# Optimization experiments

Measured on AMD Instinct MI355X. Metric: run time of the kernel, lower is better.

The kernel has to match this reference:

```python
import jax, jax.numpy as jnp
import numpy as np

N_NODES = 100000
N_EDGES = 1600000
IN_CH = 64
HID = 64
OUT = 2


def sage_conv(x, src, dst, W_agg, W_root, b):
    # PyG SAGEConv (mean aggr): out = lin_l(mean_{j in N(i)} x_j) + lin_r(x_i)
    n = x.shape[0]
    msgs = x[src]                                        # [E, F] gather
    agg = jax.ops.segment_sum(msgs, dst, num_segments=n)  # [N, F] scatter-add
    cnt = jax.ops.segment_sum(jnp.ones((src.shape[0], 1), x.dtype), dst, num_segments=n)
    agg = agg / jnp.maximum(cnt, 1)                      # mean; isolated nodes -> 0
    return agg @ W_agg + x @ W_root + b


def setup_inputs() -> dict:
    key = jax.random.key(0)
    ks = jax.random.split(key, 8)
    s = lambda f: 1.0 / np.sqrt(f)
    x = jax.random.normal(ks[0], (N_NODES, IN_CH), dtype=jnp.float32)
    edge_index = jax.random.randint(ks[1], (2, N_EDGES), 0, N_NODES, dtype=jnp.int64)
    return {
        "x": x,
        "edge_index": edge_index,
        "W1_agg": jax.random.normal(ks[2], (IN_CH, HID), dtype=jnp.float32) * s(IN_CH),
        "W1_root": jax.random.normal(ks[3], (IN_CH, HID), dtype=jnp.float32) * s(IN_CH),
        "b1": jnp.zeros((HID,), jnp.float32),
        "W2_agg": jax.random.normal(ks[4], (HID, HID), dtype=jnp.float32) * s(HID),
        "W2_root": jax.random.normal(ks[5], (HID, HID), dtype=jnp.float32) * s(HID),
        "b2": jnp.zeros((HID,), jnp.float32),
        "W_lin": jax.random.normal(ks[6], (HID, OUT), dtype=jnp.float32) * s(HID),
        "b_lin": jnp.zeros((OUT,), jnp.float32),
    }


def reference(x, edge_index, W1_agg, W1_root, b1, W2_agg, W2_root, b2, W_lin, b_lin):
    src, dst = edge_index[0], edge_index[1]
    h = jax.nn.relu(sage_conv(x, src, dst, W1_agg, W1_root, b1))   # dropout = identity (eval)
    h = jax.nn.relu(sage_conv(h, src, dst, W2_agg, W2_root, b2))
    return h @ W_lin + b_lin
```

## Files before the change

### kernel.cpp

```cpp
#include <hip/hip_runtime.h>
#include <hip/hip_bf16.h>

#define FEAT 64
#define CHUNK 8192
#define MAX_NB 1024

typedef __attribute__((ext_vector_type(8))) short bf16x8;
typedef __attribute__((ext_vector_type(4))) float f32x4;
typedef __attribute__((ext_vector_type(2))) float f32x2;

__device__ __forceinline__ float bflo2f(unsigned int u) {
    union { unsigned int u; float f; } v; v.u = u << 16; return v.f;
}
__device__ __forceinline__ float bfhi2f(unsigned int u) {
    union { unsigned int u; float f; } v; v.u = u & 0xffff0000u; return v.f;
}
__device__ __forceinline__ unsigned short f2bf(float f) {
    union { float f; unsigned int u; } v; v.f = f;
    unsigned int u = v.u;
    u += 0x7fffu + ((u >> 16) & 1u);
    return (unsigned short)(u >> 16);
}
__device__ __forceinline__ f32x2 bfpair(unsigned int u) {
    f32x2 r; r.x = bflo2f(u & 0xffffu); r.y = bfhi2f(u); return r;
}

__global__ __launch_bounds__(256) void prep_kernel(
    const unsigned short* __restrict__ xh, const int* __restrict__ ei32,
    const void* __restrict__ w1a, const void* __restrict__ w1r,
    const void* __restrict__ b1,  const void* __restrict__ w2a,
    const void* __restrict__ w2r, const void* __restrict__ b2,
    const void* __restrict__ wl,  const void* __restrict__ bl,
    float* __restrict__ wbuf, unsigned short* __restrict__ Wt,
    int* __restrict__ flags, const void* __restrict__ x_in,
    unsigned short* __restrict__ x16, int n8) {
    __shared__ int cnt_bf, cnt_nz;
    int tid = threadIdx.x;
    if (tid == 0) { cnt_bf = 0; cnt_nz = 0; }
    __syncthreads();
    unsigned short h = xh[tid * 2];
    int e = (h >> 7) & 0xFF;
    if (e >= 110 && e <= 132) atomicAdd(&cnt_bf, 1);
    if (ei32[tid * 2 + 1] != 0) atomicAdd(&cnt_nz, 1);
    __syncthreads();
    int f0 = (cnt_bf >= 128) ? 1 : 0;
    if (blockIdx.x == 0 && tid == 0) {
        flags[0] = f0;
        flags[1] = (cnt_nz < 8) ? 1 : 0;
    }
    int i = blockIdx.x * 256 + tid;
    if (i < 16642) {
        const void* src; int off;
        if      (i < 4096)  { src = w1a; off = i; }
        else if (i < 8192)  { src = w1r; off = i - 4096; }
        else if (i < 8256)  { src = b1;  off = i - 8192; }
        else if (i < 12352) { src = w2a; off = i - 8256; }
        else if (i < 16448) { src = w2r; off = i - 12352; }
        else if (i < 16512) { src = b2;  off = i - 16448; }
        else if (i < 16640) { src = wl;  off = i - 16512; }
        else                { src = bl;  off = i - 16640; }
        float v = f0 ? bflo2f(((const unsigned short*)src)[off])
                     : ((const float*)src)[off];
        wbuf[i] = v;
        unsigned short hv = f2bf(v);
        if (i < 4096)                      Wt[(off & 63) * 128 + (off >> 6)] = hv;
        else if (i < 8192)                 Wt[(off & 63) * 128 + 64 + (off >> 6)] = hv;
        else if (i >= 8256 && i < 12352)   Wt[8192 + (off & 63) * 128 + (off >> 6)] = hv;
        else if (i >= 12352 && i < 16448)  Wt[8192 + (off & 63) * 128 + 64 + (off >> 6)] = hv;
    }
    if (!f0 && i < n8) {
        float4 a = ((const float4*)x_in)[2 * i];
        float4 b = ((const float4*)x_in)[2 * i + 1];
        uint4 o;
        o.x = (unsigned int)f2bf(a.x) | ((unsigned int)f2bf(a.y) << 16);
        o.y = (unsigned int)f2bf(a.z) | ((unsigned int)f2bf(a.w) << 16);
        o.z = (unsigned int)f2bf(b.x) | ((unsigned int)f2bf(b.y) << 16);
        o.w = (unsigned int)f2bf(b.z) | ((unsigned int)f2bf(b.w) << 16);
        ((uint4*)x16)[i] = o;
    }
}

__global__ __launch_bounds__(256) void p1_hist_kernel(
    const int* __restrict__ ei32, int* __restrict__ hist,
    int E, int N, int NB, int EC, const int* __restrict__ flags) {
    __shared__ int lh[MAX_NB];
    int tid = threadIdx.x, c = blockIdx.x;
    for (int i = tid; i < NB; i += 256) lh[i] = 0;
    __syncthreads();
    int idx64 = flags[1];
    long base = (long)c * CHUNK;
#pragma unroll 4
    for (int j = 0; j < CHUNK / 256; ++j) {
        long e = base + j * 256 + tid;
        if (e < E) {
            int d = idx64 ? ei32[2 * ((long)E + e)] : ei32[(long)E + e];
            if ((unsigned)d < (unsigned)N)
                atomicAdd(&lh[d >> 8], 1);
        }
    }
    __syncthreads();
    for (int k = tid; k < NB; k += 256) hist[(long)k * EC + c] = lh[k];
}

__global__ __launch_bounds__(256) void scan1_kernel(const int* __restrict__ in,
                                                    int* __restrict__ out,
                                                    int* __restrict__ blocksum, int n) {
    int tid = threadIdx.x;
    int base = blockIdx.x * 2048 + tid * 8;
    int v[8];
    int tsum = 0;
#pragma unroll
    for (int i = 0; i < 8; ++i) {
        v[i] = (base + i < n) ? in[base + i] : 0;
        tsum += v[i];
    }
    int lane = tid & 63;
    int x = tsum;
#pragma unroll
    for (int off = 1; off < 64; off <<= 1) {
        int y = __shfl_up(x, off);
        if (lane >= off) x += y;
    }
    __shared__ int wsum[4];
    int wave = tid >> 6;
    if (lane == 63) wsum[wave] = x;
    __syncthreads();
    int woff = 0;
#pragma unroll
    for (int w = 0; w < 4; ++w) if (w < wave) woff += wsum[w];
    int run = woff + x - tsum;
#pragma unroll
    for (int i = 0; i < 8; ++i) {
        if (base + i < n) out[base + i] = run;
        run += v[i];
    }
    if (tid == 255) blocksum[blockIdx.x] = woff + x;
}

__global__ void scan3_kernel(int* __restrict__ out, const int* __restrict__ blocksum, int n) {
    int i = blockIdx.x * 256 + threadIdx.x;
    if (i >= n) return;
    int nb = i >> 11;
    int pre = 0;
    for (int b = 0; b < nb; ++b) pre += blocksum[b];
    out[i] += pre;
}

__global__ __launch_bounds__(256) void p3_scatter_kernel(
    const int* __restrict__ ei32, const int* __restrict__ hscan,
    int* __restrict__ bkt, int E, int N, int NB, int EC,
    const int* __restrict__ flags) {
    __shared__ int lh[MAX_NB];
    int tid = threadIdx.x, c = blockIdx.x;
    for (int i = tid; i < NB; i += 256) lh[i] = 0;
    __syncthreads();
    int idx64 = flags[1];
    long base = (long)c * CHUNK;
#pragma unroll 4
    for (int j = 0; j < CHUNK / 256; ++j) {
        long e = base + j * 256 + tid;
        if (e < E) {
            int s = idx64 ? ei32[2 * e]             : ei32[e];
            int d = idx64 ? ei32[2 * ((long)E + e)] : ei32[(long)E + e];
            if ((unsigned)d < (unsigned)N) {
                if ((unsigned)s >= (unsigned)N) s = 0;
                int k = d >> 8;
                int r = atomicAdd(&lh[k], 1);
                bkt[hscan[(long)k * EC + c] + r] = s | ((d & 255) << 20);
            }
        }
    }
}

__global__ __launch_bounds__(256) void p4_build_kernel(
    const int* __restrict__ bkt, const int* __restrict__ hscan, const int* __restrict__ hist,
    int* __restrict__ offs, int* __restrict__ cnt, int* __restrict__ srcs,
    int E, int N, int NB, int EC) {
    int k = blockIdx.x, tid = threadIdx.x;
    int start = hscan[(long)k * EC];
    int end = (k + 1 < NB) ? hscan[(long)(k + 1) * EC]
                           : (hscan[(long)NB * EC - 1] + hist[(long)NB * EC - 1]);
    __shared__ int lc[256], lheads[256], wsum[4];
    lc[tid] = 0;
    __syncthreads();
    for (int e = start + tid; e < end; e += 256)
        atomicAdd(&lc[(bkt[e] >> 20) & 255], 1);
    __syncthreads();
    int cv = lc[tid];
    int lane = tid & 63, wave = tid >> 6;
    int x = cv;
#pragma unroll
    for (int off = 1; off < 64; off <<= 1) {
        int y = __shfl_up(x, off);
        if (lane >= off) x += y;
    }
    if (lane == 63) wsum[wave] = x;
    __syncthreads();
    int woff = 0;
#pragma unroll
    for (int w = 0; w < 4; ++w) if (w < wave) woff += wsum[w];
    int excl = woff + x - cv;
    int gnode = k * 256 + tid;
    if (gnode < N) { offs[gnode] = start + excl; cnt[gnode] = cv; }
    lheads[tid] = excl;
    __syncthreads();
    for (int e = start + tid; e < end; e += 256) {
        int p = bkt[e];
        int d8 = (p >> 20) & 255;
        int pos = start + atomicAdd(&lheads[d8], 1);
        srcs[pos] = p & 0xFFFFF;
    }
}

__global__ __launch_bounds__(256) void sage_fused_kernel(
    const void* __restrict__ feat_raw, const unsigned short* __restrict__ feat_ws,
    const int* __restrict__ srcs, const int* __restrict__ offs,
    const int* __restrict__ cnt,
    const unsigned short* __restrict__ Wt, const float* __restrict__ bias,
    unsigned short* __restrict__ out16, int N,
    const float* __restrict__ wl, const float* __restrict__ bl,
    void* __restrict__ out_final, const int* __restrict__ flags, int sel) {

    const unsigned short* feat16 =
        (sel && !flags[0]) ? feat_ws : (const unsigned short*)feat_raw;

    __shared__ unsigned short A_l[64][136];
    __shared__ unsigned short B_l[64][136];

    int tid = threadIdx.x;
    int blk = blockIdx.x;

#pragma unroll
    for (int i = 0; i < 4; ++i) {
        int ch = tid + i * 256;
        int n = ch >> 4, kc = ch & 15;
        *(uint4*)&B_l[n][kc * 8] = *(const uint4*)(Wt + n * 128 + kc * 8);
    }
#pragma unroll
    for (int i = 0; i < 2; ++i) {
        int ch = tid + i * 256;
        int r = ch >> 3, c = ch & 7;
        int row = blk * 64 + r;
        uint4 u = make_uint4(0, 0, 0, 0);
        if (row < N) u = ((const uint4*)(feat16 + (size_t)row * FEAT))[c];
        *(uint4*)&A_l[r][64 + c * 8] = u;
    }

    int lane = tid & 63;
    int wave = tid >> 6;
    int g = lane >> 3;
    int li = lane & 7;

    for (int pass = 0; pass < 2; ++pass) {
        int r = pass * 32 + wave * 8 + g;
        int node = blk * 64 + r;
        f32x2 a0 = {0.f, 0.f}, a1 = a0, a2 = a0, a3 = a0;
        int deg = 0;
        if (node < N) {
            int start = offs[node];
            deg = cnt[node];
            int j = 0;
            for (; j + 4 <= deg; j += 4) {
                int s0 = srcs[start + j];
                int s1 = srcs[start + j + 1];
                int s2 = srcs[start + j + 2];
                int s3 = srcs[start + j + 3];
                uint4 u0 = *(const uint4*)(feat16 + (size_t)s0 * FEAT + 8 * li);
                uint4 u1 = *(const uint4*)(feat16 + (size_t)s1 * FEAT + 8 * li);
                uint4 u2 = *(const uint4*)(feat16 + (size_t)s2 * FEAT + 8 * li);
                uint4 u3 = *(const uint4*)(feat16 + (size_t)s3 * FEAT + 8 * li);
                a0 += bfpair(u0.x); a1 += bfpair(u0.y); a2 += bfpair(u0.z); a3 += bfpair(u0.w);
                a0 += bfpair(u1.x); a1 += bfpair(u1.y); a2 += bfpair(u1.z); a3 += bfpair(u1.w);
                a0 += bfpair(u2.x); a1 += bfpair(u2.y); a2 += bfpair(u2.z); a3 += bfpair(u2.w);
                a0 += bfpair(u3.x); a1 += bfpair(u3.y); a2 += bfpair(u3.z); a3 += bfpair(u3.w);
            }
            for (; j < deg; ++j) {
                int s = srcs[start + j];
                uint4 u = *(const uint4*)(feat16 + (size_t)s * FEAT + 8 * li);
                a0 += bfpair(u.x); a1 += bfpair(u.y); a2 += bfpair(u.z); a3 += bfpair(u.w);
            }
        }
        float inv = 1.0f / (float)(deg > 0 ? deg : 1);
        uint4 o;
        o.x = (unsigned)f2bf(a0.x * inv) | ((unsigned)f2bf(a0.y * inv) << 16);
        o.y = (unsigned)f2bf(a1.x * inv) | ((unsigned)f2bf(a1.y * inv) << 16);
        o.z = (unsigned)f2bf(a2.x * inv) | ((unsigned)f2bf(a2.y * inv) << 16);
        o.w = (unsigned)f2bf(a3.x * inv) | ((unsigned)f2bf(a3.y * inv) << 16);
        *(uint4*)&A_l[r][8 * li] = o;
    }
    __syncthreads();

    int r0 = wave * 16;
    int m = lane & 15, quad = lane >> 4;

    f32x4 acc0 = {0.f, 0.f, 0.f, 0.f};
    f32x4 acc1 = acc0, acc2 = acc0, acc3 = acc0;

#pragma unroll
    for (int k0 = 0; k0 < 128; k0 += 32) {
        bf16x8 a = *(const bf16x8*)&A_l[r0 + m][k0 + quad * 8];
        bf16x8 b0 = *(const bf16x8*)&B_l[ 0 + m][k0 + quad * 8];
        bf16x8 b1 = *(const bf16x8*)&B_l[16 + m][k0 + quad * 8];
        bf16x8 b2 = *(const bf16x8*)&B_l[32 + m][k0 + quad * 8];
        bf16x8 b3 = *(const bf16x8*)&B_l[48 + m][k0 + quad * 8];
        acc0 = __builtin_amdgcn_mfma_f32_16x16x32_bf16(a, b0, acc0, 0, 0, 0);
        acc1 = __builtin_amdgcn_mfma_f32_16x16x32_bf16(a, b1, acc1, 0, 0, 0);
        acc2 = __builtin_amdgcn_mfma_f32_16x16x32_bf16(a, b2, acc2, 0, 0, 0);
        acc3 = __builtin_amdgcn_mfma_f32_16x16x32_bf16(a, b3, acc3, 0, 0, 0);
    }
    __syncthreads();

#pragma unroll
    for (int c = 0; c < 4; ++c) {
        f32x4 av = (c == 0) ? acc0 : (c == 1) ? acc1 : (c == 2) ? acc2 : acc3;
        float bv = bias[c * 16 + m];
#pragma unroll
        for (int reg = 0; reg < 4; ++reg) {
            float v = fmaxf(av[reg] + bv, 0.f);
            A_l[r0 + quad * 4 + reg][c * 16 + m] = f2bf(v);
        }
    }
    __syncthreads();

    if (out16) {
#pragma unroll
        for (int i = 0; i < 2; ++i) {
            int ch = tid + i * 256;
            int r = ch >> 3, c = ch & 7;
            int row = blk * 64 + r;
            if (row < N)
                ((uint4*)(out16 + (size_t)row * FEAT))[c] = *(const uint4*)&A_l[r][c * 8];
        }
    }

    if (wl) {
        int r = tid >> 2, part = tid & 3;
        int row = blk * 64 + r;
        if (row < N) {
            float p0 = 0.f, p1 = 0.f;
#pragma unroll
            for (int j = 0; j < 16; ++j) {
                int f = part * 16 + j;
                float v = bflo2f(A_l[r][f]);
                p0 += v * wl[f * 2 + 0];
                p1 += v * wl[f * 2 + 1];
            }
            p0 += __shfl_down(p0, 2, 4); p0 += __shfl_down(p0, 1, 4);
            p1 += __shfl_down(p1, 2, 4); p1 += __shfl_down(p1, 1, 4);
            if (part == 0) {
                p0 += bl[0];
                p1 += bl[1];
                if (flags[0]) {
                    unsigned int o = ((unsigned int)f2bf(p1) << 16) | (unsigned int)f2bf(p0);
                    ((unsigned int*)out_final)[row] = o;
                } else {
                    ((float2*)out_final)[row] = make_float2(p0, p1);
                }
            }
        }
    }
}

extern "C" void kernel_launch(void* const* d_in, const int* in_sizes, int n_in,
                              void* d_out, int out_size, void* d_ws, size_t ws_size,
                              hipStream_t stream) {
    const void* x_in = d_in[0];
    const int*  ei32 = (const int*)d_in[1];

    int N = in_sizes[0] / FEAT;
    int E = in_sizes[1] / 2;
    int NB = (N + 255) >> 8;
    int EC = (E + CHUNK - 1) / CHUNK;
    int HN = NB * EC;

    unsigned short* x16   = (unsigned short*)d_ws;
    unsigned short* h16   = x16 + (size_t)N * FEAT;
    unsigned short* Wt    = h16 + (size_t)N * FEAT;
    float*          wbuf  = (float*)(Wt + 16384);
    int*            hist  = (int*)(wbuf + 16704);
    int*            hscan = hist + HN;
    int*            bsum  = hscan + HN;
    int*            flags = bsum + 1024;
    int*            offs  = flags + 16;
    int*            cnt   = offs + N;
    int*            bkt   = cnt + N;
    int*            srcs  = bkt + E;

    float* b1_32 = wbuf + 8192;
    float* b2_32 = wbuf + 16448;
    float* wl32  = wbuf + 16512;
    float* bl32  = wbuf + 16640;

    int n8 = N * FEAT / 8;
    int pBlocks = (n8 + 255) / 256;
    if (pBlocks < 66) pBlocks = 66;
    prep_kernel<<<pBlocks, 256, 0, stream>>>(
        (const unsigned short*)x_in, ei32,
        d_in[2], d_in[3], d_in[4], d_in[5], d_in[6], d_in[7], d_in[8], d_in[9],
        wbuf, Wt, flags, x_in, x16, n8);

    p1_hist_kernel<<<EC, 256, 0, stream>>>(ei32, hist, E, N, NB, EC, flags);
    int sB = (HN + 2047) / 2048;
    scan1_kernel<<<sB, 256, 0, stream>>>(hist, hscan, bsum, HN);
    scan3_kernel<<<(HN + 255) / 256, 256, 0, stream>>>(hscan, bsum, HN);
    p3_scatter_kernel<<<EC, 256, 0, stream>>>(ei32, hscan, bkt, E, N, NB, EC, flags);
    p4_build_kernel<<<NB, 256, 0, stream>>>(bkt, hscan, hist, offs, cnt, srcs, E, N, NB, EC);

    int gBlocks = (N + 63) / 64;

    sage_fused_kernel<<<gBlocks, 256, 0, stream>>>(
        x_in, x16, srcs, offs, cnt, Wt, b1_32, h16, N,
        nullptr, nullptr, nullptr, flags, 1);

    sage_fused_kernel<<<gBlocks, 256, 0, stream>>>(
        h16, h16, srcs, offs, cnt, Wt + 8192, b2_32, nullptr, N,
        wl32, bl32, d_out, flags, 0);
}
```

Before: 233.9 us.

## Stage neighbor indices in LDS, read weights from global, and rework the scan

The fused SAGE kernel no longer stages the weight tile in shared memory. It reads the B operands for MFMA straight from global/L2 and uses the freed LDS to hold the block's contiguous neighbor-index range, with a global fallback when the range overflows. Launch bounds now request 6 blocks per SM to raise occupancy for the latency-bound gather. Separately, the scan fixup kernel runs one block per 2048-element segment and sums prefixes in parallel rather than looping serially per thread. CHUNK drops to 2048, which changes the edge-chunk count and histogram sizes for the sort phases.

```diff
diff --git a/kernel.cpp b/kernel.cpp
--- a/kernel.cpp
+++ b/kernel.cpp
@@ -2,8 +2,9 @@
 #include <hip/hip_bf16.h>
 
 #define FEAT 64
-#define CHUNK 8192
+#define CHUNK 2048
 #define MAX_NB 1024
+#define SCAP 1792
 
 typedef __attribute__((ext_vector_type(8))) short bf16x8;
 typedef __attribute__((ext_vector_type(4))) float f32x4;
@@ -137,13 +138,27 @@
     if (tid == 255) blocksum[blockIdx.x] = woff + x;
 }
 
-__global__ void scan3_kernel(int* __restrict__ out, const int* __restrict__ blocksum, int n) {
-    int i = blockIdx.x * 256 + threadIdx.x;
-    if (i >= n) return;
-    int nb = i >> 11;
-    int pre = 0;
-    for (int b = 0; b < nb; ++b) pre += blocksum[b];
-    out[i] += pre;
+__global__ __launch_bounds__(256) void scan3_kernel(int* __restrict__ out,
+                                                    const int* __restrict__ blocksum, int n) {
+    int bb = blockIdx.x, tid = threadIdx.x;
+    __shared__ int wsum[4];
+    __shared__ int spre;
+    int s = 0;
+    for (int b = tid; b < bb; b += 256) s += blocksum[b];
+#pragma unroll
+    for (int off = 32; off > 0; off >>= 1) s += __shfl_down(s, off);
+    int lane = tid & 63, wave = tid >> 6;
+    if (lane == 0) wsum[wave] = s;
+    __syncthreads();
+    if (tid == 0) spre = wsum[0] + wsum[1] + wsum[2] + wsum[3];
+    __syncthreads();
+    int pre = spre;
+    int base = bb * 2048;
+#pragma unroll
+    for (int k = 0; k < 8; ++k) {
+        int i = base + k * 256 + tid;
+        if (i < n) out[i] += pre;
+    }
 }
 
 __global__ __launch_bounds__(256) void p3_scatter_kernel(
@@ -212,7 +227,7 @@
     }
 }
 
-__global__ __launch_bounds__(256) void sage_fused_kernel(
+__global__ __launch_bounds__(256, 6) void sage_fused_kernel(
     const void* __restrict__ feat_raw, const unsigned short* __restrict__ feat_ws,
     const int* __restrict__ srcs, const int* __restrict__ offs,
     const int* __restrict__ cnt,
@@ -225,17 +240,18 @@
         (sel && !flags[0]) ? feat_ws : (const unsigned short*)feat_raw;
 
     __shared__ unsigned short A_l[64][136];
-    __shared__ unsigned short B_l[64][136];
+    __shared__ int srcs_l[SCAP];
 
     int tid = threadIdx.x;
     int blk = blockIdx.x;
 
-#pragma unroll
-    for (int i = 0; i < 4; ++i) {
-        int ch = tid + i * 256;
-        int n = ch >> 4, kc = ch & 15;
-        *(uint4*)&B_l[n][kc * 8] = *(const uint4*)(Wt + n * 128 + kc * 8);
-    }
+    int first = blk * 64;
+    int lastN = first + 63; if (lastN >= N) lastN = N - 1;
+    int eb = offs[first];
+    int eEnd = offs[lastN] + cnt[lastN];
+    int nE = eEnd - eb; if (nE > SCAP) nE = SCAP;
+    for (int i = tid; i < nE; i += 256) srcs_l[i] = srcs[eb + i];
+
 #pragma unroll
     for (int i = 0; i < 2; ++i) {
         int ch = tid + i * 256;
@@ -245,6 +261,7 @@
         if (row < N) u = ((const uint4*)(feat16 + (size_t)row * FEAT))[c];
         *(uint4*)&A_l[r][64 + c * 8] = u;
     }
+    __syncthreads();
 
     int lane = tid & 63;
     int wave = tid >> 6;
@@ -259,25 +276,49 @@
         if (node < N) {
             int start = offs[node];
             deg = cnt[node];
-            int j = 0;
-            for (; j + 4 <= deg; j += 4) {
-                int s0 = srcs[start + j];
-                int s1 = srcs[start + j + 1];
-                int s2 = srcs[start + j + 2];
-                int s3 = srcs[start + j + 3];
-                uint4 u0 = *(const uint4*)(feat16 + (size_t)s0 * FEAT + 8 * li);
-                uint4 u1 = *(const uint4*)(feat16 + (size_t)s1 * FEAT + 8 * li);
-                uint4 u2 = *(const uint4*)(feat16 + (size_t)s2 * FEAT + 8 * li);
-                uint4 u3 = *(const uint4*)(feat16 + (size_t)s3 * FEAT + 8 * li);
-                a0 += bfpair(u0.x); a1 += bfpair(u0.y); a2 += bfpair(u0.z); a3 += bfpair(u0.w);
-                a0 += bfpair(u1.x); a1 += bfpair(u1.y); a2 += bfpair(u1.z); a3 += bfpair(u1.w);
-                a0 += bfpair(u2.x); a1 += bfpair(u2.y); a2 += bfpair(u2.z); a3 += bfpair(u2.w);
-                a0 += bfpair(u3.x); a1 += bfpair(u3.y); a2 += bfpair(u3.z); a3 += bfpair(u3.w);
-            }
-            for (; j < deg; ++j) {
-                int s = srcs[start + j];
-                uint4 u = *(const uint4*)(feat16 + (size_t)s * FEAT + 8 * li);
-                a0 += bfpair(u.x); a1 += bfpair(u.y); a2 += bfpair(u.z); a3 += bfpair(u.w);
+            int base = start - eb;
+            if (base + deg <= SCAP) {
+                int j = 0;
+                for (; j + 4 <= deg; j += 4) {
+                    int s0 = srcs_l[base + j];
+                    int s1 = srcs_l[base + j + 1];
+                    int s2 = srcs_l[base + j + 2];
+                    int s3 = srcs_l[base + j + 3];
+                    uint4 u0 = *(const uint4*)(feat16 + (size_t)s0 * FEAT + 8 * li);
+                    uint4 u1 = *(const uint4*)(feat16 + (size_t)s1 * FEAT + 8 * li);
+                    uint4 u2 = *(const uint4*)(feat16 + (size_t)s2 * FEAT + 8 * li);
+                    uint4 u3 = *(const uint4*)(feat16 + (size_t)s3 * FEAT + 8 * li);
+                    a0 += bfpair(u0.x); a1 += bfpair(u0.y); a2 += bfpair(u0.z); a3 += bfpair(u0.w);
+                    a0 += bfpair(u1.x); a1 += bfpair(u1.y); a2 += bfpair(u1.z); a3 += bfpair(u1.w);
+                    a0 += bfpair(u2.x); a1 += bfpair(u2.y); a2 += bfpair(u2.z); a3 += bfpair(u2.w);
+                    a0 += bfpair(u3.x); a1 += bfpair(u3.y); a2 += bfpair(u3.z); a3 += bfpair(u3.w);
+                }
+                for (; j < deg; ++j) {
+                    int s = srcs_l[base + j];
+                    uint4 u = *(const uint4*)(feat16 + (size_t)s * FEAT + 8 * li);
+                    a0 += bfpair(u.x); a1 += bfpair(u.y); a2 += bfpair(u.z); a3 += bfpair(u.w);
+                }
+            } else {
+                int j = 0;
+                for (; j + 4 <= deg; j += 4) {
+                    int s0 = srcs[start + j];
+                    int s1 = srcs[start + j + 1];
+                    int s2 = srcs[start + j + 2];
+                    int s3 = srcs[start + j + 3];
+                    uint4 u0 = *(const uint4*)(feat16 + (size_t)s0 * FEAT + 8 * li);
+                    uint4 u1 = *(const uint4*)(feat16 + (size_t)s1 * FEAT + 8 * li);
+                    uint4 u2 = *(const uint4*)(feat16 + (size_t)s2 * FEAT + 8 * li);
+                    uint4 u3 = *(const uint4*)(feat16 + (size_t)s3 * FEAT + 8 * li);
+                    a0 += bfpair(u0.x); a1 += bfpair(u0.y); a2 += bfpair(u0.z); a3 += bfpair(u0.w);
+                    a0 += bfpair(u1.x); a1 += bfpair(u1.y); a2 += bfpair(u1.z); a3 += bfpair(u1.w);
+                    a0 += bfpair(u2.x); a1 += bfpair(u2.y); a2 += bfpair(u2.z); a3 += bfpair(u2.w);
+                    a0 += bfpair(u3.x); a1 += bfpair(u3.y); a2 += bfpair(u3.z); a3 += bfpair(u3.w);
+                }
+                for (; j < deg; ++j) {
+                    int s = srcs[start + j];
+                    uint4 u = *(const uint4*)(feat16 + (size_t)s * FEAT + 8 * li);
+                    a0 += bfpair(u.x); a1 += bfpair(u.y); a2 += bfpair(u.z); a3 += bfpair(u.w);
+                }
             }
         }
         float inv = 1.0f / (float)(deg > 0 ? deg : 1);
@@ -298,11 +339,11 @@
 
 #pragma unroll
     for (int k0 = 0; k0 < 128; k0 += 32) {
-        bf16x8 a = *(const bf16x8*)&A_l[r0 + m][k0 + quad * 8];
-        bf16x8 b0 = *(const bf16x8*)&B_l[ 0 + m][k0 + quad * 8];
-        bf16x8 b1 = *(const bf16x8*)&B_l[16 + m][k0 + quad * 8];
-        bf16x8 b2 = *(const bf16x8*)&B_l[32 + m][k0 + quad * 8];
-        bf16x8 b3 = *(const bf16x8*)&B_l[48 + m][k0 + quad * 8];
+        bf16x8 a  = *(const bf16x8*)&A_l[r0 + m][k0 + quad * 8];
+        bf16x8 b0 = *(const bf16x8*)(Wt + ( 0 + m) * 128 + k0 + quad * 8);
+        bf16x8 b1 = *(const bf16x8*)(Wt + (16 + m) * 128 + k0 + quad * 8);
+        bf16x8 b2 = *(const bf16x8*)(Wt + (32 + m) * 128 + k0 + quad * 8);
+        bf16x8 b3 = *(const bf16x8*)(Wt + (48 + m) * 128 + k0 + quad * 8);
         acc0 = __builtin_amdgcn_mfma_f32_16x16x32_bf16(a, b0, acc0, 0, 0, 0);
         acc1 = __builtin_amdgcn_mfma_f32_16x16x32_bf16(a, b1, acc1, 0, 0, 0);
         acc2 = __builtin_amdgcn_mfma_f32_16x16x32_bf16(a, b2, acc2, 0, 0, 0);
@@ -402,7 +443,7 @@
     p1_hist_kernel<<<EC, 256, 0, stream>>>(ei32, hist, E, N, NB, EC, flags);
     int sB = (HN + 2047) / 2048;
     scan1_kernel<<<sB, 256, 0, stream>>>(hist, hscan, bsum, HN);
-    scan3_kernel<<<(HN + 255) / 256, 256, 0, stream>>>(hscan, bsum, HN);
+    scan3_kernel<<<sB, 256, 0, stream>>>(hscan, bsum, HN);
     p3_scatter_kernel<<<EC, 256, 0, stream>>>(ei32, hscan, bkt, E, N, NB, EC, flags);
     p4_build_kernel<<<NB, 256, 0, stream>>>(bkt, hscan, hist, offs, cnt, srcs, E, N, NB, EC);
 
```

Result: slower. 240.7 us (+2.9%).

## Fuse histogram into prep kernel, shrink chunks, parallelize scan3, load root features directly

Applied to the files above, without the earlier changes.

Merges the edge histogram pass into the prep kernel launch by appending extra blocks that each compute their own index-width flag, which removes one kernel launch and lets histogramming overlap with the weight and feature conversion. It shrinks the edge chunk size so more blocks take part in the histogram and scatter passes. It rewrites scan3 so each block reduces its prefix once and adds it to 2048 outputs, instead of every thread looping serially over block sums. The fused SAGE kernel now reads root-node features straight from global memory into the MFMA operand instead of staging them in shared memory. That halves the A tile's LDS footprint but adds uncoalesced global loads inside the MMA loop.

```diff
diff --git a/kernel.cpp b/kernel.cpp
--- a/kernel.cpp
+++ b/kernel.cpp
@@ -2,7 +2,7 @@
 #include <hip/hip_bf16.h>
 
 #define FEAT 64
-#define CHUNK 8192
+#define CHUNK 2048
 #define MAX_NB 1024
 
 typedef __attribute__((ext_vector_type(8))) short bf16x8;
@@ -25,7 +25,7 @@
     f32x2 r; r.x = bflo2f(u & 0xffffu); r.y = bfhi2f(u); return r;
 }
 
-__global__ __launch_bounds__(256) void prep_kernel(
+__global__ __launch_bounds__(256) void prep_p1_kernel(
     const unsigned short* __restrict__ xh, const int* __restrict__ ei32,
     const void* __restrict__ w1a, const void* __restrict__ w1r,
     const void* __restrict__ b1,  const void* __restrict__ w2a,
@@ -33,9 +33,35 @@
     const void* __restrict__ wl,  const void* __restrict__ bl,
     float* __restrict__ wbuf, unsigned short* __restrict__ Wt,
     int* __restrict__ flags, const void* __restrict__ x_in,
-    unsigned short* __restrict__ x16, int n8) {
+    unsigned short* __restrict__ x16, int n8,
+    int* __restrict__ hist, int E, int N, int NB, int EC, int pB) {
+    __shared__ int lh[MAX_NB];
     __shared__ int cnt_bf, cnt_nz;
     int tid = threadIdx.x;
+
+    if (blockIdx.x >= pB) {
+        int c = blockIdx.x - pB;
+        if (tid == 0) cnt_nz = 0;
+        for (int i = tid; i < NB; i += 256) lh[i] = 0;
+        __syncthreads();
+        if (ei32[tid * 2 + 1] != 0) atomicAdd(&cnt_nz, 1);
+        __syncthreads();
+        int idx64 = (cnt_nz < 8) ? 1 : 0;
+        long base = (long)c * CHUNK;
+#pragma unroll 4
+        for (int j = 0; j < CHUNK / 256; ++j) {
+            long e = base + j * 256 + tid;
+            if (e < E) {
+                int d = idx64 ? ei32[2 * ((long)E + e)] : ei32[(long)E + e];
+                if ((unsigned)d < (unsigned)N)
+                    atomicAdd(&lh[d >> 8], 1);
+            }
+        }
+        __syncthreads();
+        for (int k = tid; k < NB; k += 256) hist[(long)k * EC + c] = lh[k];
+        return;
+    }
+
     if (tid == 0) { cnt_bf = 0; cnt_nz = 0; }
     __syncthreads();
     unsigned short h = xh[tid * 2];
@@ -80,28 +106,6 @@
     }
 }
 
-__global__ __launch_bounds__(256) void p1_hist_kernel(
-    const int* __restrict__ ei32, int* __restrict__ hist,
-    int E, int N, int NB, int EC, const int* __restrict__ flags) {
-    __shared__ int lh[MAX_NB];
-    int tid = threadIdx.x, c = blockIdx.x;
-    for (int i = tid; i < NB; i += 256) lh[i] = 0;
-    __syncthreads();
-    int idx64 = flags[1];
-    long base = (long)c * CHUNK;
-#pragma unroll 4
-    for (int j = 0; j < CHUNK / 256; ++j) {
-        long e = base + j * 256 + tid;
-        if (e < E) {
-            int d = idx64 ? ei32[2 * ((long)E + e)] : ei32[(long)E + e];
-            if ((unsigned)d < (unsigned)N)
-                atomicAdd(&lh[d >> 8], 1);
-        }
-    }
-    __syncthreads();
-    for (int k = tid; k < NB; k += 256) hist[(long)k * EC + c] = lh[k];
-}
-
 __global__ __launch_bounds__(256) void scan1_kernel(const int* __restrict__ in,
                                                     int* __restrict__ out,
                                                     int* __restrict__ blocksum, int n) {
@@ -137,13 +141,27 @@
     if (tid == 255) blocksum[blockIdx.x] = woff + x;
 }
 
-__global__ void scan3_kernel(int* __restrict__ out, const int* __restrict__ blocksum, int n) {
-    int i = blockIdx.x * 256 + threadIdx.x;
-    if (i >= n) return;
-    int nb = i >> 11;
-    int pre = 0;
-    for (int b = 0; b < nb; ++b) pre += blocksum[b];
-    out[i] += pre;
+__global__ __launch_bounds__(256) void scan3_kernel(int* __restrict__ out,
+                                                    const int* __restrict__ blocksum, int n) {
+    int bb = blockIdx.x, tid = threadIdx.x;
+    __shared__ int wsum[4];
+    __shared__ int spre;
+    int s = 0;
+    for (int b = tid; b < bb; b += 256) s += blocksum[b];
+#pragma unroll
+    for (int off = 32; off > 0; off >>= 1) s += __shfl_down(s, off);
+    int lane = tid & 63, wave = tid >> 6;
+    if (lane == 0) wsum[wave] = s;
+    __syncthreads();
+    if (tid == 0) spre = wsum[0] + wsum[1] + wsum[2] + wsum[3];
+    __syncthreads();
+    int pre = spre;
+    int base = bb * 2048;
+#pragma unroll
+    for (int k = 0; k < 8; ++k) {
+        int i = base + k * 256 + tid;
+        if (i < n) out[i] += pre;
+    }
 }
 
 __global__ __launch_bounds__(256) void p3_scatter_kernel(
@@ -224,7 +242,7 @@
     const unsigned short* feat16 =
         (sel && !flags[0]) ? feat_ws : (const unsigned short*)feat_raw;
 
-    __shared__ unsigned short A_l[64][136];
+    __shared__ unsigned short A_l[64][72];
     __shared__ unsigned short B_l[64][136];
 
     int tid = threadIdx.x;
@@ -235,15 +253,6 @@
         int ch = tid + i * 256;
         int n = ch >> 4, kc = ch & 15;
         *(uint4*)&B_l[n][kc * 8] = *(const uint4*)(Wt + n * 128 + kc * 8);
-    }
-#pragma unroll
-    for (int i = 0; i < 2; ++i) {
-        int ch = tid + i * 256;
-        int r = ch >> 3, c = ch & 7;
-        int row = blk * 64 + r;
-        uint4 u = make_uint4(0, 0, 0, 0);
-        if (row < N) u = ((const uint4*)(feat16 + (size_t)row * FEAT))[c];
-        *(uint4*)&A_l[r][64 + c * 8] = u;
     }
 
     int lane = tid & 63;
@@ -293,12 +302,18 @@
     int r0 = wave * 16;
     int m = lane & 15, quad = lane >> 4;
 
+    int arow = blk * 64 + r0 + m;
+    if (arow >= N) arow = 0;
+    const unsigned short* rootp = feat16 + (size_t)arow * FEAT + quad * 8;
+
     f32x4 acc0 = {0.f, 0.f, 0.f, 0.f};
     f32x4 acc1 = acc0, acc2 = acc0, acc3 = acc0;
 
 #pragma unroll
     for (int k0 = 0; k0 < 128; k0 += 32) {
-        bf16x8 a = *(const bf16x8*)&A_l[r0 + m][k0 + quad * 8];
+        bf16x8 a;
+        if (k0 < 64) a = *(const bf16x8*)&A_l[r0 + m][k0 + quad * 8];
+        else         a = *(const bf16x8*)(rootp + (k0 - 64));
         bf16x8 b0 = *(const bf16x8*)&B_l[ 0 + m][k0 + quad * 8];
         bf16x8 b1 = *(const bf16x8*)&B_l[16 + m][k0 + quad * 8];
         bf16x8 b2 = *(const bf16x8*)&B_l[32 + m][k0 + quad * 8];
@@ -394,15 +409,15 @@
     int n8 = N * FEAT / 8;
     int pBlocks = (n8 + 255) / 256;
     if (pBlocks < 66) pBlocks = 66;
-    prep_kernel<<<pBlocks, 256, 0, stream>>>(
+    prep_p1_kernel<<<pBlocks + EC, 256, 0, stream>>>(
         (const unsigned short*)x_in, ei32,
         d_in[2], d_in[3], d_in[4], d_in[5], d_in[6], d_in[7], d_in[8], d_in[9],
-        wbuf, Wt, flags, x_in, x16, n8);
-
-    p1_hist_kernel<<<EC, 256, 0, stream>>>(ei32, hist, E, N, NB, EC, flags);
+        wbuf, Wt, flags, x_in, x16, n8,
+        hist, E, N, NB, EC, pBlocks);
+
     int sB = (HN + 2047) / 2048;
     scan1_kernel<<<sB, 256, 0, stream>>>(hist, hscan, bsum, HN);
-    scan3_kernel<<<(HN + 255) / 256, 256, 0, stream>>>(hscan, bsum, HN);
+    scan3_kernel<<<sB, 256, 0, stream>>>(hscan, bsum, HN);
     p3_scatter_kernel<<<EC, 256, 0, stream>>>(ei32, hscan, bkt, E, N, NB, EC, flags);
     p4_build_kernel<<<NB, 256, 0, stream>>>(bkt, hscan, hist, offs, cnt, srcs, E, N, NB, EC);
 
```

Result: no change. 231.4 us (median of 2 runs) (-1.1%).
